# Performance work log

Hardware: AMD Instinct MI355X
Metric: run time of the kernel (lower is better)

Reference implementation:

```python
import jax, jax.numpy as jnp
import numpy as np

B, S, D = 8, 1024, 1024
H = 16
D_HEAD = D // H
RANK = 256
NC = 64
NE = 64
KC = 16  # top_k_compress
KE = 8   # top_k_expand


def setup_inputs() -> dict:
    key = jax.random.key(0)
    ks = jax.random.split(key, 9)
    rn = lambda k, sh, s=1.0: jax.random.normal(k, sh, jnp.float32) * s
    return {
        "x": rn(ks[0], (B, S, D)),
        "importance": jax.random.uniform(ks[1], (B, S), jnp.float32),
        "W_compress": rn(ks[2], (NC, D), 1.0 / np.sqrt(D)),
        "W_Q": rn(ks[3], (NE, D), 1.0 / np.sqrt(D)),
        "W_K": rn(ks[4], (NE, D), 1.0 / np.sqrt(D)),
        "W_V": rn(ks[5], (NE, D), 1.0 / np.sqrt(D)),
        "compress_neurons": rn(ks[6], (NC, D, RANK), 1.0 / np.sqrt(D)),
        "expand_pool": rn(ks[7], (NE, RANK, D), 1.0 / np.sqrt(RANK)),
        "W_O": rn(ks[8], (D, D), 1.0 / np.sqrt(D)),
    }


def _route(x, importance, W, k):
    """Per-token softmax router, importance-aggregated, top-k renormalized."""
    pref = jax.nn.softmax(jnp.einsum('bsd,nd->bsn', x, W), axis=-1)  # [B,S,n]
    w = jnp.einsum('bs,bsn->bn', importance, pref)                   # [B,n]
    w = w / (w.sum(-1, keepdims=True) + 1e-8)
    tw, ti = jax.lax.top_k(w, k)                                     # [B,k]
    tw = tw / (tw.sum(-1, keepdims=True) + 1e-8)
    return tw, ti


def reference(x, importance, W_compress, W_Q, W_K, W_V, compress_neurons, expand_pool, W_O):
    # --- GlobalRouters.get_attention_weights ---
    cw, ci = _route(x, importance, W_compress, KC)
    qw, qi = _route(x, importance, W_Q, KE)
    kw, ki = _route(x, importance, W_K, KE)
    vw, vi = _route(x, importance, W_V, KE)

    # --- NeuronCircuit.forward ---
    # gather + mix compress neurons: [B,KC,D,R] -> [B,D,R]
    shared_c = jnp.einsum('bk,bkdr->bdr', cw, compress_neurons[ci])
    h = jnp.einsum('bsd,bdr->bsr', x, shared_c)  # [B,S,R]

    eQ = jnp.einsum('bk,bkrd->brd', qw, expand_pool[qi])
    eK = jnp.einsum('bk,bkrd->brd', kw, expand_pool[ki])
    eV = jnp.einsum('bk,bkrd->brd', vw, expand_pool[vi])

    def heads(t):  # [B,S,D] -> [B,H,S,d_head]
        return t.reshape(B, S, H, D_HEAD).transpose(0, 2, 1, 3)

    Q = heads(jnp.einsum('bsr,brd->bsd', h, eQ))
    K = heads(jnp.einsum('bsr,brd->bsd', h, eK))
    V = heads(jnp.einsum('bsr,brd->bsd', h, eV))

    scale = 1.0 / np.sqrt(D_HEAD)
    scores = jnp.einsum('bhqd,bhkd->bhqk', Q, K) * scale
    causal = jnp.tril(jnp.ones((S, S), dtype=bool))
    scores = jnp.where(causal, scores, jnp.finfo(scores.dtype).min)
    attn = jax.nn.softmax(scores, axis=-1)
    out = jnp.einsum('bhqk,bhkd->bhqd', attn, V)
    out = out.transpose(0, 2, 1, 3).reshape(B, S, D)
    return jnp.einsum('bsd,ed->bse', out, W_O)  # expand_O (Linear, no bias)
```

## Files before the change

kernel.cpp:

```cpp
#include <hip/hip_runtime.h>

typedef __attribute__((ext_vector_type(8))) short short8;
typedef __attribute__((ext_vector_type(4))) short short4v;
typedef __attribute__((ext_vector_type(4))) float f32x4;
typedef unsigned short u16;
typedef unsigned int u32;

__device__ __forceinline__ float bf2f(u16 h) {
    return __uint_as_float(((u32)h) << 16);
}
__device__ __forceinline__ u16 f2bf(float f) {
    u32 u = __float_as_uint(f);
    u32 r = u + 0x7fffu + ((u >> 16) & 1u);
    return (u16)(r >> 16);
}
__device__ __forceinline__ u32 pack_bf(float a, float b) {
    return __builtin_amdgcn_perm(__float_as_uint(b), __float_as_uint(a), 0x07060302u);
}

__device__ __forceinline__ void async_copy16(const void* g, void* l) {
    __builtin_amdgcn_global_load_lds(
        (const __attribute__((address_space(1))) void*)g,
        (__attribute__((address_space(3))) void*)l, 16, 0, 0);
}

__global__ __launch_bounds__(256) void cvt_split(
    const float* __restrict__ in, u16* __restrict__ hi, u16* __restrict__ lo, int n4)
{
    int i = blockIdx.x * 256 + threadIdx.x;
    if (i >= n4) return;
    float4 v = ((const float4*)in)[i];
    short4v h, l;
    float vv[4] = {v.x, v.y, v.z, v.w};
#pragma unroll
    for (int j = 0; j < 4; j++) {
        u16 hb = f2bf(vv[j]);
        h[j] = (short)hb;
        l[j] = (short)f2bf(vv[j] - bf2f(hb));
    }
    ((short4v*)hi)[i] = h;
    ((short4v*)lo)[i] = l;
}

__global__ __launch_bounds__(256) void cvt_split_w4(
    const float* __restrict__ w0, const float* __restrict__ w1,
    const float* __restrict__ w2, const float* __restrict__ w3,
    u16* __restrict__ hi, u16* __restrict__ lo)
{
    const int r = blockIdx.x >> 6;
    const float* src = (r == 0) ? w0 : (r == 1) ? w1 : (r == 2) ? w2 : w3;
    int i = (blockIdx.x & 63) * 256 + threadIdx.x;
    float4 v = ((const float4*)src)[i];
    short4v h, l;
    float vv[4] = {v.x, v.y, v.z, v.w};
#pragma unroll
    for (int j = 0; j < 4; j++) {
        u16 hb = f2bf(vv[j]);
        h[j] = (short)hb;
        l[j] = (short)f2bf(vv[j] - bf2f(hb));
    }
    ((short4v*)(hi + (long)r * 65536))[i] = h;
    ((short4v*)(lo + (long)r * 65536))[i] = l;
}

__global__ __launch_bounds__(256) void cvt_bf(
    const float* __restrict__ in, u16* __restrict__ out, int n4)
{
    int i = blockIdx.x * 256 + threadIdx.x;
    if (i >= n4) return;
    float4 v = ((const float4*)in)[i];
    short4v h;
    h[0] = (short)f2bf(v.x); h[1] = (short)f2bf(v.y);
    h[2] = (short)f2bf(v.z); h[3] = (short)f2bf(v.w);
    ((short4v*)out)[i] = h;
}

template <typename CT>
__global__ __launch_bounds__(256) void gemm_bt(
    const u16* __restrict__ A, long lda, long bsA,
    const u16* __restrict__ Bm, long ldb, long bsB,
    CT* __restrict__ C, long ldc, long bsC, int K, float cscale)
{
    __shared__ __align__(16) u16 lsA[128 * 32];
    __shared__ __align__(16) u16 lsB[128 * 32];
    const int tid = threadIdx.x;
    const int wave = tid >> 6, lane = tid & 63;
    const int quad = lane >> 4, l15 = lane & 15;
    const int wm = wave >> 1, wn = wave & 1;
    const long m0 = (long)blockIdx.x * 128, n0 = (long)blockIdx.y * 128;
    A  += (long)blockIdx.z * bsA;
    Bm += (long)blockIdx.z * bsB;
    C  += (long)blockIdx.z * bsC;
    const int srow = lane >> 2, scol = (lane & 3) * 8;

    f32x4 acc[4][4];
#pragma unroll
    for (int i = 0; i < 4; i++)
#pragma unroll
        for (int j = 0; j < 4; j++) acc[i][j] = (f32x4){0.f, 0.f, 0.f, 0.f};

    const u16* ga0 = A + (m0 + (wave * 2 + 0) * 16 + srow) * lda + scol;
    const u16* ga1 = A + (m0 + (wave * 2 + 1) * 16 + srow) * lda + scol;
    const u16* gb0 = Bm + (n0 + (wave * 2 + 0) * 16 + srow) * ldb + scol;
    const u16* gb1 = Bm + (n0 + (wave * 2 + 1) * 16 + srow) * ldb + scol;
    u16* la0 = &lsA[(wave * 2 + 0) * 512];
    u16* la1 = &lsA[(wave * 2 + 1) * 512];
    u16* lb0 = &lsB[(wave * 2 + 0) * 512];
    u16* lb1 = &lsB[(wave * 2 + 1) * 512];

    for (int kk = 0; kk < K; kk += 32) {
        async_copy16(ga0 + kk, la0);
        async_copy16(ga1 + kk, la1);
        async_copy16(gb0 + kk, lb0);
        async_copy16(gb1 + kk, lb1);
        __syncthreads();
        short8 af[4], bf[4];
#pragma unroll
        for (int mt = 0; mt < 4; mt++)
            af[mt] = *(const short8*)&lsA[(wm * 64 + mt * 16 + l15) * 32 + quad * 8];
#pragma unroll
        for (int nt = 0; nt < 4; nt++)
            bf[nt] = *(const short8*)&lsB[(wn * 64 + nt * 16 + l15) * 32 + quad * 8];
#pragma unroll
        for (int mt = 0; mt < 4; mt++)
#pragma unroll
            for (int nt = 0; nt < 4; nt++)
                acc[mt][nt] = __builtin_amdgcn_mfma_f32_16x16x32_bf16(
                    af[mt], bf[nt], acc[mt][nt], 0, 0, 0);
        __syncthreads();
    }
#pragma unroll
    for (int mt = 0; mt < 4; mt++) {
        const long rowb = m0 + wm * 64 + mt * 16 + quad * 4;
#pragma unroll
        for (int nt = 0; nt < 4; nt++) {
            const long col = n0 + wn * 64 + nt * 16 + l15;
#pragma unroll
            for (int r = 0; r < 4; r++) {
                const float v = acc[mt][nt][r] * cscale;
                if constexpr (sizeof(CT) == 2)
                    C[(rowb + r) * ldc + col] = f2bf(v);
                else
                    C[(rowb + r) * ldc + col] = v;
            }
        }
    }
}

__global__ __launch_bounds__(256) void gemm_qkv(
    const u16* __restrict__ hbuf, const u16* __restrict__ eQT,
    const u16* __restrict__ eKT, const u16* __restrict__ eVT,
    u16* __restrict__ Qb, u16* __restrict__ Kb, u16* __restrict__ VTb)
{
    __shared__ __align__(16) u16 lsA[128 * 32];
    __shared__ __align__(16) u16 lsB[128 * 32];
    const int z = blockIdx.z;
    const int sel = z >> 3, bbz = z & 7;
    const long ab = (long)bbz * 262144;
    const u16* A  = ((sel == 2) ? eVT : hbuf) + ab;
    const u16* Bm = ((sel == 0) ? eQT : (sel == 1) ? eKT : hbuf) + ab;
    u16* C = ((sel == 0) ? Qb : (sel == 1) ? Kb : VTb) + (long)bbz * 1048576;
    const float cscale = (sel == 0) ? 0.180336880111f : 1.0f;

    const int tid = threadIdx.x;
    const int wave = tid >> 6, lane = tid & 63;
    const int quad = lane >> 4, l15 = lane & 15;
    const int wm = wave >> 1, wn = wave & 1;
    const long m0 = (long)blockIdx.x * 128, n0 = (long)blockIdx.y * 128;
    const int srow = lane >> 2, scol = (lane & 3) * 8;

    f32x4 acc[4][4];
#pragma unroll
    for (int i = 0; i < 4; i++)
#pragma unroll
        for (int j = 0; j < 4; j++) acc[i][j] = (f32x4){0.f, 0.f, 0.f, 0.f};

    const u16* ga0 = A + (m0 + (wave * 2 + 0) * 16 + srow) * 256 + scol;
    const u16* ga1 = A + (m0 + (wave * 2 + 1) * 16 + srow) * 256 + scol;
    const u16* gb0 = Bm + (n0 + (wave * 2 + 0) * 16 + srow) * 256 + scol;
    const u16* gb1 = Bm + (n0 + (wave * 2 + 1) * 16 + srow) * 256 + scol;
    u16* la0 = &lsA[(wave * 2 + 0) * 512];
    u16* la1 = &lsA[(wave * 2 + 1) * 512];
    u16* lb0 = &lsB[(wave * 2 + 0) * 512];
    u16* lb1 = &lsB[(wave * 2 + 1) * 512];

    for (int kk = 0; kk < 256; kk += 32) {
        async_copy16(ga0 + kk, la0);
        async_copy16(ga1 + kk, la1);
        async_copy16(gb0 + kk, lb0);
        async_copy16(gb1 + kk, lb1);
        __syncthreads();
        short8 af[4], bf[4];
#pragma unroll
        for (int mt = 0; mt < 4; mt++)
            af[mt] = *(const short8*)&lsA[(wm * 64 + mt * 16 + l15) * 32 + quad * 8];
#pragma unroll
        for (int nt = 0; nt < 4; nt++)
            bf[nt] = *(const short8*)&lsB[(wn * 64 + nt * 16 + l15) * 32 + quad * 8];
#pragma unroll
        for (int mt = 0; mt < 4; mt++)
#pragma unroll
            for (int nt = 0; nt < 4; nt++)
                acc[mt][nt] = __builtin_amdgcn_mfma_f32_16x16x32_bf16(
                    af[mt], bf[nt], acc[mt][nt], 0, 0, 0);
        __syncthreads();
    }
#pragma unroll
    for (int mt = 0; mt < 4; mt++) {
        const long rowb = m0 + wm * 64 + mt * 16 + quad * 4;
#pragma unroll
        for (int nt = 0; nt < 4; nt++) {
            const long col = n0 + wn * 64 + nt * 16 + l15;
#pragma unroll
            for (int r = 0; r < 4; r++)
                C[(rowb + r) * 1024 + col] = f2bf(acc[mt][nt][r] * cscale);
        }
    }
}

__global__ __launch_bounds__(256) void gemm_router(
    const u16* __restrict__ Ah, const u16* __restrict__ Al,
    const u16* __restrict__ Bh, const u16* __restrict__ Bl,
    float* __restrict__ C)
{
    __shared__ __align__(16) u16 lsA[128 * 32];
    __shared__ __align__(16) u16 lsB[128 * 32];
    const int tid = threadIdx.x;
    const int wave = tid >> 6, lane = tid & 63;
    const int quad = lane >> 4, l15 = lane & 15;
    const int wm = wave >> 1, wn = wave & 1;
    const long m0 = (long)blockIdx.x * 128, n0 = (long)blockIdx.y * 128;
    const int srow = lane >> 2, scol = (lane & 3) * 8;
    const long offA = (m0 + (wave * 2) * 16 + srow) * 1024 + scol;
    const long offB = (n0 + (wave * 2) * 16 + srow) * 1024 + scol;
    u16* la0 = &lsA[(wave * 2 + 0) * 512];
    u16* la1 = &lsA[(wave * 2 + 1) * 512];
    u16* lb0 = &lsB[(wave * 2 + 0) * 512];
    u16* lb1 = &lsB[(wave * 2 + 1) * 512];

    f32x4 acc[4][4];
#pragma unroll
    for (int i = 0; i < 4; i++)
#pragma unroll
        for (int j = 0; j < 4; j++) acc[i][j] = (f32x4){0.f, 0.f, 0.f, 0.f};

    for (int seg = 0; seg < 3; seg++) {
        const u16* A = (seg == 1) ? Al : Ah;
        const u16* B = (seg == 2) ? Bl : Bh;
        const u16* ga = A + offA;
        const u16* gb = B + offB;
        for (int kk = 0; kk < 1024; kk += 32) {
            async_copy16(ga + kk, la0);
            async_copy16(ga + 16384 + kk, la1);
            async_copy16(gb + kk, lb0);
            async_copy16(gb + 16384 + kk, lb1);
            __syncthreads();
            short8 af[4], bf[4];
#pragma unroll
            for (int mt = 0; mt < 4; mt++)
                af[mt] = *(const short8*)&lsA[(wm * 64 + mt * 16 + l15) * 32 + quad * 8];
#pragma unroll
            for (int nt = 0; nt < 4; nt++)
                bf[nt] = *(const short8*)&lsB[(wn * 64 + nt * 16 + l15) * 32 + quad * 8];
#pragma unroll
            for (int mt = 0; mt < 4; mt++)
#pragma unroll
                for (int nt = 0; nt < 4; nt++)
                    acc[mt][nt] = __builtin_amdgcn_mfma_f32_16x16x32_bf16(
                        af[mt], bf[nt], acc[mt][nt], 0, 0, 0);
            __syncthreads();
        }
    }
#pragma unroll
    for (int mt = 0; mt < 4; mt++) {
        const long rowb = m0 + wm * 64 + mt * 16 + quad * 4;
#pragma unroll
        for (int nt = 0; nt < 4; nt++) {
            const long col = n0 + wn * 64 + nt * 16 + l15;
#pragma unroll
            for (int r = 0; r < 4; r++)
                C[(rowb + r) * 256 + col] = acc[mt][nt][r];
        }
    }
}

__global__ __launch_bounds__(128) void router_agg(
    const float* __restrict__ logits, const float* __restrict__ imp,
    float* __restrict__ w_raw)
{
    __shared__ float pref[32][257];
    const int tid = threadIdx.x;
    const int tl = tid >> 2, r = tid & 3;
    const int s = blockIdx.x * 32 + tl;
    const int b = s >> 10;
    const float* lp = logits + (long)s * 256 + r * 64;
    float v[64];
#pragma unroll
    for (int i = 0; i < 16; i++) {
        float4 f = ((const float4*)lp)[i];
        v[i * 4 + 0] = f.x; v[i * 4 + 1] = f.y;
        v[i * 4 + 2] = f.z; v[i * 4 + 3] = f.w;
    }
    float mx = v[0];
#pragma unroll
    for (int i = 1; i < 64; i++) mx = fmaxf(mx, v[i]);
    float sum = 0.f;
#pragma unroll
    for (int i = 0; i < 64; i++) { v[i] = __expf(v[i] - mx); sum += v[i]; }
    const float scale = imp[s] / sum;
#pragma unroll
    for (int i = 0; i < 64; i++) pref[tl][r * 64 + i] = v[i] * scale;
    __syncthreads();
#pragma unroll
    for (int half = 0; half < 2; half++) {
        const int idx = tid + half * 128;
        const int r2 = idx >> 6, n = idx & 63;
        float acc = 0.f;
#pragma unroll 8
        for (int t = 0; t < 32; t++) acc += pref[t][r2 * 64 + n];
        atomicAdd(&w_raw[(r2 * 8 + b) * 64 + n], acc);
    }
}

__global__ void topk_kernel(const float* __restrict__ w_raw,
                            float* __restrict__ topw, int* __restrict__ topi)
{
    const int r = blockIdx.x >> 3, b = blockIdx.x & 7;
    const int lane = threadIdx.x;
    const int k = (r == 0) ? 16 : 8;
    float w = w_raw[(r * 8 + b) * 64 + lane];
    float tot = w;
    for (int o2 = 32; o2 >= 1; o2 >>= 1) tot += __shfl_xor(tot, o2);
    w = w / (tot + 1e-8f);
    __shared__ float tw[16];
    __shared__ int ti[16];
    float cur = w;
    float ssum = 0.f;
    for (int j = 0; j < k; j++) {
        float m = cur; int mi = lane;
        for (int o2 = 32; o2 >= 1; o2 >>= 1) {
            float om = __shfl_xor(m, o2); int oi = __shfl_xor(mi, o2);
            if (om > m || (om == m && oi < mi)) { m = om; mi = oi; }
        }
        if (lane == 0) { tw[j] = m; ti[j] = mi; }
        ssum += m;
        if (lane == mi) cur = -1e30f;
    }
    __syncthreads();
    if (lane < 16) {
        topw[(r * 8 + b) * 16 + lane] = (lane < k) ? tw[lane] / (ssum + 1e-8f) : 0.f;
        topi[(r * 8 + b) * 16 + lane] = (lane < k) ? ti[lane] : 0;
    }
}

__global__ __launch_bounds__(256) void gather_mix(
    const float* __restrict__ pool, const float* __restrict__ topw,
    const int* __restrict__ topi, u16* __restrict__ out,
    int I, int J, int k)
{
    __shared__ float tile[64][65];
    const int b = blockIdx.z;
    const long IJ = (long)I * J;
    const int i0 = blockIdx.x * 64, j0 = blockIdx.y * 64;
    const float* tw = topw + b * 16;
    const int* ti = topi + b * 16;
    const int tid = threadIdx.x;
    const int il = tid >> 2, jg = tid & 3;
    float acc[16];
#pragma unroll
    for (int m = 0; m < 16; m++) acc[m] = 0.f;
    for (int kk = 0; kk < k; kk++) {
        const float wgt = tw[kk];
        const long n = ti[kk];
        const float* src = pool + n * IJ + (long)(i0 + il) * J + j0 + jg * 16;
        float4 a0 = ((const float4*)src)[0];
        float4 a1 = ((const float4*)src)[1];
        float4 a2 = ((const float4*)src)[2];
        float4 a3 = ((const float4*)src)[3];
        acc[0] += wgt * a0.x;  acc[1] += wgt * a0.y;
        acc[2] += wgt * a0.z;  acc[3] += wgt * a0.w;
        acc[4] += wgt * a1.x;  acc[5] += wgt * a1.y;
        acc[6] += wgt * a1.z;  acc[7] += wgt * a1.w;
        acc[8] += wgt * a2.x;  acc[9] += wgt * a2.y;
        acc[10] += wgt * a2.z; acc[11] += wgt * a2.w;
        acc[12] += wgt * a3.x; acc[13] += wgt * a3.y;
        acc[14] += wgt * a3.z; acc[15] += wgt * a3.w;
    }
#pragma unroll
    for (int m = 0; m < 16; m++) tile[il][jg * 16 + m] = acc[m];
    __syncthreads();
    const int jl = tid >> 2, ig = tid & 3;
    short8 o0, o1;
#pragma unroll
    for (int m = 0; m < 8; m++) {
        o0[m] = (short)f2bf(tile[ig * 16 + m][jl]);
        o1[m] = (short)f2bf(tile[ig * 16 + 8 + m][jl]);
    }
    u16* dst = out + (long)b * IJ + (long)(j0 + jl) * I + i0 + ig * 16;
    *(short8*)dst = o0;
    *(short8*)(dst + 8) = o1;
}

__global__ __launch_bounds__(256) void gather_mix3(
    const float* __restrict__ pool, const float* __restrict__ topw,
    const int* __restrict__ topi, u16* __restrict__ eQT,
    u16* __restrict__ eKT, u16* __restrict__ eVT)
{
    __shared__ float tile[64][65];
    const int z = blockIdx.z;
    const int r = z >> 3, b = z & 7;
    u16* out = (r == 0) ? eQT : (r == 1) ? eKT : eVT;
    const long IJ = 262144;
    const int i0 = blockIdx.x * 64, j0 = blockIdx.y * 64;
    const float* tw = topw + (1 + r) * 128 + b * 16;
    const int* ti = topi + (1 + r) * 128 + b * 16;
    const int tid = threadIdx.x;
    const int il = tid >> 2, jg = tid & 3;
    float acc[16];
#pragma unroll
    for (int m = 0; m < 16; m++) acc[m] = 0.f;
    for (int kk = 0; kk < 8; kk++) {
        const float wgt = tw[kk];
        const long n = ti[kk];
        const float* src = pool + n * IJ + (long)(i0 + il) * 1024 + j0 + jg * 16;
        float4 a0 = ((const float4*)src)[0];
        float4 a1 = ((const float4*)src)[1];
        float4 a2 = ((const float4*)src)[2];
        float4 a3 = ((const float4*)src)[3];
        acc[0] += wgt * a0.x;  acc[1] += wgt * a0.y;
        acc[2] += wgt * a0.z;  acc[3] += wgt * a0.w;
        acc[4] += wgt * a1.x;  acc[5] += wgt * a1.y;
        acc[6] += wgt * a1.z;  acc[7] += wgt * a1.w;
        acc[8] += wgt * a2.x;  acc[9] += wgt * a2.y;
        acc[10] += wgt * a2.z; acc[11] += wgt * a2.w;
        acc[12] += wgt * a3.x; acc[13] += wgt * a3.y;
        acc[14] += wgt * a3.z; acc[15] += wgt * a3.w;
    }
#pragma unroll
    for (int m = 0; m < 16; m++) tile[il][jg * 16 + m] = acc[m];
    __syncthreads();
    const int jl = tid >> 2, ig = tid & 3;
    short8 o0, o1;
#pragma unroll
    for (int m = 0; m < 8; m++) {
        o0[m] = (short)f2bf(tile[ig * 16 + m][jl]);
        o1[m] = (short)f2bf(tile[ig * 16 + 8 + m][jl]);
    }
    u16* dst = out + (long)b * IJ + (long)(j0 + jl) * 256 + i0 + ig * 16;
    *(short8*)dst = o0;
    *(short8*)(dst + 8) = o1;
}

__global__ __launch_bounds__(256, 3) void flash_attn(
    const u16* __restrict__ Qg, const u16* __restrict__ Kg,
    const u16* __restrict__ Vt, u16* __restrict__ Og)
{
    __shared__ __align__(16) u16 plds[4][32 * 72];
    const int tid = threadIdx.x;
    const int wv = tid >> 6, lane = tid & 63;
    const int quad = lane >> 4, l15 = lane & 15;
    const int bidx = blockIdx.x;
    const int bh = bidx & 127;
    const int qt = ((7 - (bidx >> 7)) << 2) + wv;
    const int hh = bh & 15, bb = bh >> 4;
    const long SD = 1024L * 1024L;
    const u16* Qb = Qg + (long)bb * SD + hh * 64;
    const u16* Kb = Kg + (long)bb * SD + hh * 64;
    const u16* Vb = Vt + (long)bb * SD + (long)hh * 64 * 1024;
    u16* myp = plds[wv];

    const int q0 = qt * 32;

    short8 qf[2][2];
#pragma unroll
    for (int mt = 0; mt < 2; mt++)
#pragma unroll
        for (int kb = 0; kb < 2; kb++)
            qf[mt][kb] = *(const short8*)(Qb + (long)(q0 + mt * 16 + l15) * 1024 + kb * 32 + quad * 8);

    f32x4 o[2][4];
    float mrow[2] = {-3e38f, -3e38f}, lrow[2] = {0.f, 0.f};
#pragma unroll
    for (int mt = 0; mt < 2; mt++)
#pragma unroll
        for (int nt = 0; nt < 4; nt++) o[mt][nt] = (f32x4){0.f, 0.f, 0.f, 0.f};

    const int ntile = (q0 + 95) >> 6;

    for (int it = 0; it < ntile; it++) {
        const int k2 = it * 64;
        const bool last = (it == ntile - 1);
        short8 kf[4][2];
#pragma unroll
        for (int kt = 0; kt < 4; kt++)
#pragma unroll
            for (int kb = 0; kb < 2; kb++)
                kf[kt][kb] = *(const short8*)(Kb + (long)(k2 + kt * 16 + l15) * 1024 + kb * 32 + quad * 8);
        f32x4 st[4][2];
#pragma unroll
        for (int kt = 0; kt < 4; kt++)
#pragma unroll
            for (int q_ = 0; q_ < 2; q_++) {
                f32x4 z = (f32x4){0.f, 0.f, 0.f, 0.f};
                z = __builtin_amdgcn_mfma_f32_16x16x32_bf16(kf[kt][0], qf[q_][0], z, 0, 0, 0);
                z = __builtin_amdgcn_mfma_f32_16x16x32_bf16(kf[kt][1], qf[q_][1], z, 0, 0, 0);
                st[kt][q_] = z;
            }
        short8 vf[4][2];
#pragma unroll
        for (int nt = 0; nt < 4; nt++)
#pragma unroll
            for (int kh = 0; kh < 2; kh++)
                vf[nt][kh] = *(const short8*)(Vb + (long)(nt * 16 + l15) * 1024 + k2 + kh * 32 + quad * 8);
        float am[2];
#pragma unroll
        for (int q_ = 0; q_ < 2; q_++) {
            if (last) {
#pragma unroll
                for (int kt = 0; kt < 4; kt++)
#pragma unroll
                    for (int r = 0; r < 4; r++)
                        if (k2 + kt * 16 + quad * 4 + r > q0 + q_ * 16 + l15)
                            st[kt][q_][r] = -3e38f;
            }
            float cm = -3e38f;
#pragma unroll
            for (int kt = 0; kt < 4; kt++)
#pragma unroll
                for (int r = 0; r < 4; r++) cm = fmaxf(cm, st[kt][q_][r]);
            cm = fmaxf(cm, __shfl_xor(cm, 16));
            cm = fmaxf(cm, __shfl_xor(cm, 32));
            const float mn = fmaxf(mrow[q_], cm);
            am[q_] = exp2f(mrow[q_] - mn);
            mrow[q_] = mn;
            const float moff = 0.00281502f - mn;
            float rs = 0.f;
#pragma unroll
            for (int kt = 0; kt < 4; kt++) {
                float p0 = exp2f(st[kt][q_][0] + moff);
                float p1 = exp2f(st[kt][q_][1] + moff);
                float p2 = exp2f(st[kt][q_][2] + moff);
                float p3 = exp2f(st[kt][q_][3] + moff);
                rs += (p0 + p1) + (p2 + p3);
                u32 w0 = pack_bf(p0, p1);
                u32 w1 = pack_bf(p2, p3);
                *(uint2*)&myp[(q_ * 16 + l15) * 72 + kt * 16 + quad * 4] = make_uint2(w0, w1);
            }
            rs += __shfl_xor(rs, 16);
            rs += __shfl_xor(rs, 32);
            lrow[q_] = lrow[q_] * am[q_] + rs;
        }
        float av[2][4];
#pragma unroll
        for (int mt = 0; mt < 2; mt++)
#pragma unroll
            for (int r = 0; r < 4; r++)
                av[mt][r] = __shfl(am[mt], quad * 4 + r);
        asm volatile("s_waitcnt lgkmcnt(0)" ::: "memory");
        short8 pf0[2], pf1[2];
#pragma unroll
        for (int kh = 0; kh < 2; kh++) {
            pf0[kh] = *(const short8*)&myp[(l15) * 72 + kh * 32 + quad * 8];
            pf1[kh] = *(const short8*)&myp[(16 + l15) * 72 + kh * 32 + quad * 8];
        }
#pragma unroll
        for (int mt = 0; mt < 2; mt++)
#pragma unroll
            for (int nt = 0; nt < 4; nt++)
#pragma unroll
                for (int r = 0; r < 4; r++) o[mt][nt][r] *= av[mt][r];
#pragma unroll
        for (int nt = 0; nt < 4; nt++)
#pragma unroll
            for (int kh = 0; kh < 2; kh++) {
                o[0][nt] = __builtin_amdgcn_mfma_f32_16x16x32_bf16(pf0[kh], vf[nt][kh], o[0][nt], 0, 0, 0);
                o[1][nt] = __builtin_amdgcn_mfma_f32_16x16x32_bf16(pf1[kh], vf[nt][kh], o[1][nt], 0, 0, 0);
            }
    }
#pragma unroll
    for (int mt = 0; mt < 2; mt++)
#pragma unroll
        for (int r = 0; r < 4; r++) {
            const float li = 1.0f / __shfl(lrow[mt], quad * 4 + r);
            const long row = q0 + mt * 16 + quad * 4 + r;
#pragma unroll
            for (int nt = 0; nt < 4; nt++)
                Og[(long)bb * SD + row * 1024 + hh * 64 + nt * 16 + l15] =
                    f2bf(o[mt][nt][r] * li);
        }
}

extern "C" void kernel_launch(void* const* d_in, const int* in_sizes, int n_in,
                              void* d_out, int out_size, void* d_ws, size_t ws_size,
                              hipStream_t stream)
{
    const float* x   = (const float*)d_in[0];
    const float* imp = (const float*)d_in[1];
    const float* cn  = (const float*)d_in[6];
    const float* ep  = (const float*)d_in[7];
    const float* Wo  = (const float*)d_in[8];
    float* outp = (float*)d_out;
    char* ws = (char*)d_ws;

    u16* xh = (u16*)d_out;
    u16* xl = xh + 8388608;

    u16*   Wh     = (u16*)(ws + 0);
    u16*   Wl     = (u16*)(ws + 524288);
    u16*   Wobf   = (u16*)(ws + 1048576);
    float* w_raw  = (float*)(ws + 3145728);
    float* topw   = (float*)(ws + 3153920);
    int*   topi   = (int*)(ws + 3155968);
    float* logits = (float*)(ws + 4194304);
    u16*   scT    = (u16*)(ws + 12582912);
    u16*   eQT    = (u16*)(ws + 16777216);
    u16*   Kb     = (u16*)(ws + 4194304);
    u16*   hbuf   = (u16*)(ws + 20971520);
    u16*   eKT    = (u16*)(ws + 25165824);
    u16*   eVT    = (u16*)(ws + 29360128);
    u16*   Qb     = (u16*)(ws + 33554432);
    u16*   VTb    = (u16*)(ws + 50331648);
    u16*   aout   = (u16*)(ws + 67108864);

    cvt_split<<<dim3(8192), 256, 0, stream>>>(x, xh, xl, 2097152);
    cvt_split_w4<<<dim3(256), 256, 0, stream>>>(
        (const float*)d_in[2], (const float*)d_in[3],
        (const float*)d_in[4], (const float*)d_in[5], Wh, Wl);
    cvt_bf<<<dim3(1024), 256, 0, stream>>>(Wo, Wobf, 262144);
    hipMemsetAsync(w_raw, 0, 4 * 8 * 64 * 4, stream);

    gemm_router<<<dim3(64, 2, 1), 256, 0, stream>>>(xh, xl, Wh, Wl, logits);
    router_agg<<<dim3(256), 128, 0, stream>>>(logits, imp, w_raw);
    topk_kernel<<<dim3(32), 64, 0, stream>>>(w_raw, topw, topi);
    gather_mix<<<dim3(16, 4, 8), 256, 0, stream>>>(cn, topw + 0 * 128, topi + 0 * 128, scT, 1024, 256, 16);
    gather_mix3<<<dim3(4, 16, 24), 256, 0, stream>>>(ep, topw, topi, eQT, eKT, eVT);
    gemm_bt<u16><<<dim3(8, 2, 8), 256, 0, stream>>>(
        xh, 1024, 1048576, scT, 1024, 262144, hbuf, 256, 262144, 1024, 1.0f);
    gemm_qkv<<<dim3(8, 8, 24), 256, 0, stream>>>(hbuf, eQT, eKT, eVT, Qb, Kb, VTb);
    flash_attn<<<dim3(1024), 256, 0, stream>>>(Qb, Kb, VTb, aout);
    gemm_bt<float><<<dim3(64, 8, 1), 256, 0, stream>>>(
        aout, 1024, 0, Wobf, 1024, 0, outp, 1024, 0, 1024, 1.0f);
}
```

Baseline: 448.2 us.

## Split router GEMM segments across blocks and keep attention P in registers

The three split-precision router GEMM passes now run as separate grid slices along z, writing three partial logit buffers that router_agg sums. This triples the number of blocks for a grid that was only 128 blocks, at the cost of extra logit memory traffic. Flash attention now prefetches the next K tile during the current tile's compute, builds the P operand with cross-lane shuffles instead of an LDS round trip, and uses a tree reduction for the row max. These changes target latency and LDS traffic in the attention loop and add shuffle instructions and register pressure in exchange.

Result: no change. 439.5 us (-2.0%).

```diff
diff --git a/kernel.cpp b/kernel.cpp
--- a/kernel.cpp
+++ b/kernel.cpp
@@ -5,6 +5,7 @@
 typedef __attribute__((ext_vector_type(4))) float f32x4;
 typedef unsigned short u16;
 typedef unsigned int u32;
+typedef __attribute__((ext_vector_type(4))) u32 u32x4;
 
 __device__ __forceinline__ float bf2f(u16 h) {
     return __uint_as_float(((u32)h) << 16);
@@ -16,6 +17,10 @@
 }
 __device__ __forceinline__ u32 pack_bf(float a, float b) {
     return __builtin_amdgcn_perm(__float_as_uint(b), __float_as_uint(a), 0x07060302u);
+}
+__device__ __forceinline__ short8 u4_to_s8(u32 a, u32 b, u32 c, u32 d) {
+    u32x4 t = (u32x4){a, b, c, d};
+    return __builtin_bit_cast(short8, t);
 }
 
 __device__ __forceinline__ void async_copy16(const void* g, void* l) {
@@ -221,18 +226,22 @@
 __global__ __launch_bounds__(256) void gemm_router(
     const u16* __restrict__ Ah, const u16* __restrict__ Al,
     const u16* __restrict__ Bh, const u16* __restrict__ Bl,
-    float* __restrict__ C)
+    float* __restrict__ C0, float* __restrict__ C1, float* __restrict__ C2)
 {
     __shared__ __align__(16) u16 lsA[128 * 32];
     __shared__ __align__(16) u16 lsB[128 * 32];
+    const int seg = blockIdx.z;
+    const u16* A = (seg == 1) ? Al : Ah;
+    const u16* B = (seg == 2) ? Bl : Bh;
+    float* C = (seg == 0) ? C0 : (seg == 1) ? C1 : C2;
     const int tid = threadIdx.x;
     const int wave = tid >> 6, lane = tid & 63;
     const int quad = lane >> 4, l15 = lane & 15;
     const int wm = wave >> 1, wn = wave & 1;
     const long m0 = (long)blockIdx.x * 128, n0 = (long)blockIdx.y * 128;
     const int srow = lane >> 2, scol = (lane & 3) * 8;
-    const long offA = (m0 + (wave * 2) * 16 + srow) * 1024 + scol;
-    const long offB = (n0 + (wave * 2) * 16 + srow) * 1024 + scol;
+    const u16* ga = A + (m0 + (wave * 2) * 16 + srow) * 1024 + scol;
+    const u16* gb = B + (n0 + (wave * 2) * 16 + srow) * 1024 + scol;
     u16* la0 = &lsA[(wave * 2 + 0) * 512];
     u16* la1 = &lsA[(wave * 2 + 1) * 512];
     u16* lb0 = &lsB[(wave * 2 + 0) * 512];
@@ -244,32 +253,26 @@
 #pragma unroll
         for (int j = 0; j < 4; j++) acc[i][j] = (f32x4){0.f, 0.f, 0.f, 0.f};
 
-    for (int seg = 0; seg < 3; seg++) {
-        const u16* A = (seg == 1) ? Al : Ah;
-        const u16* B = (seg == 2) ? Bl : Bh;
-        const u16* ga = A + offA;
-        const u16* gb = B + offB;
-        for (int kk = 0; kk < 1024; kk += 32) {
-            async_copy16(ga + kk, la0);
-            async_copy16(ga + 16384 + kk, la1);
-            async_copy16(gb + kk, lb0);
-            async_copy16(gb + 16384 + kk, lb1);
-            __syncthreads();
-            short8 af[4], bf[4];
-#pragma unroll
-            for (int mt = 0; mt < 4; mt++)
-                af[mt] = *(const short8*)&lsA[(wm * 64 + mt * 16 + l15) * 32 + quad * 8];
+    for (int kk = 0; kk < 1024; kk += 32) {
+        async_copy16(ga + kk, la0);
+        async_copy16(ga + 16384 + kk, la1);
+        async_copy16(gb + kk, lb0);
+        async_copy16(gb + 16384 + kk, lb1);
+        __syncthreads();
+        short8 af[4], bf[4];
+#pragma unroll
+        for (int mt = 0; mt < 4; mt++)
+            af[mt] = *(const short8*)&lsA[(wm * 64 + mt * 16 + l15) * 32 + quad * 8];
+#pragma unroll
+        for (int nt = 0; nt < 4; nt++)
+            bf[nt] = *(const short8*)&lsB[(wn * 64 + nt * 16 + l15) * 32 + quad * 8];
+#pragma unroll
+        for (int mt = 0; mt < 4; mt++)
 #pragma unroll
             for (int nt = 0; nt < 4; nt++)
-                bf[nt] = *(const short8*)&lsB[(wn * 64 + nt * 16 + l15) * 32 + quad * 8];
-#pragma unroll
-            for (int mt = 0; mt < 4; mt++)
-#pragma unroll
-                for (int nt = 0; nt < 4; nt++)
-                    acc[mt][nt] = __builtin_amdgcn_mfma_f32_16x16x32_bf16(
-                        af[mt], bf[nt], acc[mt][nt], 0, 0, 0);
-            __syncthreads();
-        }
+                acc[mt][nt] = __builtin_amdgcn_mfma_f32_16x16x32_bf16(
+                    af[mt], bf[nt], acc[mt][nt], 0, 0, 0);
+        __syncthreads();
     }
 #pragma unroll
     for (int mt = 0; mt < 4; mt++) {
@@ -285,7 +288,8 @@
 }
 
 __global__ __launch_bounds__(128) void router_agg(
-    const float* __restrict__ logits, const float* __restrict__ imp,
+    const float* __restrict__ l0, const float* __restrict__ l1,
+    const float* __restrict__ l2, const float* __restrict__ imp,
     float* __restrict__ w_raw)
 {
     __shared__ float pref[32][257];
@@ -293,13 +297,17 @@
     const int tl = tid >> 2, r = tid & 3;
     const int s = blockIdx.x * 32 + tl;
     const int b = s >> 10;
-    const float* lp = logits + (long)s * 256 + r * 64;
+    const long off = (long)s * 256 + r * 64;
     float v[64];
 #pragma unroll
     for (int i = 0; i < 16; i++) {
-        float4 f = ((const float4*)lp)[i];
-        v[i * 4 + 0] = f.x; v[i * 4 + 1] = f.y;
-        v[i * 4 + 2] = f.z; v[i * 4 + 3] = f.w;
+        float4 f0 = ((const float4*)(l0 + off))[i];
+        float4 f1 = ((const float4*)(l1 + off))[i];
+        float4 f2 = ((const float4*)(l2 + off))[i];
+        v[i * 4 + 0] = f0.x + f1.x + f2.x;
+        v[i * 4 + 1] = f0.y + f1.y + f2.y;
+        v[i * 4 + 2] = f0.z + f1.z + f2.z;
+        v[i * 4 + 3] = f0.w + f1.w + f2.w;
     }
     float mx = v[0];
 #pragma unroll
@@ -455,7 +463,6 @@
     const u16* __restrict__ Qg, const u16* __restrict__ Kg,
     const u16* __restrict__ Vt, u16* __restrict__ Og)
 {
-    __shared__ __align__(16) u16 plds[4][32 * 72];
     const int tid = threadIdx.x;
     const int wv = tid >> 6, lane = tid & 63;
     const int quad = lane >> 4, l15 = lane & 15;
@@ -467,7 +474,6 @@
     const u16* Qb = Qg + (long)bb * SD + hh * 64;
     const u16* Kb = Kg + (long)bb * SD + hh * 64;
     const u16* Vb = Vt + (long)bb * SD + (long)hh * 64 * 1024;
-    u16* myp = plds[wv];
 
     const int q0 = qt * 32;
 
@@ -486,16 +492,20 @@
         for (int nt = 0; nt < 4; nt++) o[mt][nt] = (f32x4){0.f, 0.f, 0.f, 0.f};
 
     const int ntile = (q0 + 95) >> 6;
+    short8 kf[4][2];
+#pragma unroll
+    for (int kt = 0; kt < 4; kt++)
+#pragma unroll
+        for (int kb = 0; kb < 2; kb++)
+            kf[kt][kb] = *(const short8*)(Kb + (long)(kt * 16 + l15) * 1024 + kb * 32 + quad * 8);
+
+    const int sl01 = l15 + ((((quad << 1) + 0) & 3) << 4);
+    const int sl23 = l15 + ((((quad << 1) + 1) & 3) << 4);
+    const bool loquad = (quad < 2);
 
     for (int it = 0; it < ntile; it++) {
         const int k2 = it * 64;
         const bool last = (it == ntile - 1);
-        short8 kf[4][2];
-#pragma unroll
-        for (int kt = 0; kt < 4; kt++)
-#pragma unroll
-            for (int kb = 0; kb < 2; kb++)
-                kf[kt][kb] = *(const short8*)(Kb + (long)(k2 + kt * 16 + l15) * 1024 + kb * 32 + quad * 8);
         f32x4 st[4][2];
 #pragma unroll
         for (int kt = 0; kt < 4; kt++)
@@ -506,6 +516,13 @@
                 z = __builtin_amdgcn_mfma_f32_16x16x32_bf16(kf[kt][1], qf[q_][1], z, 0, 0, 0);
                 st[kt][q_] = z;
             }
+        if (it + 1 < ntile) {
+#pragma unroll
+            for (int kt = 0; kt < 4; kt++)
+#pragma unroll
+                for (int kb = 0; kb < 2; kb++)
+                    kf[kt][kb] = *(const short8*)(Kb + (long)(k2 + 64 + kt * 16 + l15) * 1024 + kb * 32 + quad * 8);
+        }
         short8 vf[4][2];
 #pragma unroll
         for (int nt = 0; nt < 4; nt++)
@@ -513,6 +530,7 @@
             for (int kh = 0; kh < 2; kh++)
                 vf[nt][kh] = *(const short8*)(Vb + (long)(nt * 16 + l15) * 1024 + k2 + kh * 32 + quad * 8);
         float am[2];
+        u32 pa[2][2][4];
 #pragma unroll
         for (int q_ = 0; q_ < 2; q_++) {
             if (last) {
@@ -523,32 +541,42 @@
                         if (k2 + kt * 16 + quad * 4 + r > q0 + q_ * 16 + l15)
                             st[kt][q_][r] = -3e38f;
             }
-            float cm = -3e38f;
-#pragma unroll
-            for (int kt = 0; kt < 4; kt++)
-#pragma unroll
-                for (int r = 0; r < 4; r++) cm = fmaxf(cm, st[kt][q_][r]);
+            float t0 = fmaxf(fmaxf(st[0][q_][0], st[0][q_][1]), fmaxf(st[0][q_][2], st[0][q_][3]));
+            float t1 = fmaxf(fmaxf(st[1][q_][0], st[1][q_][1]), fmaxf(st[1][q_][2], st[1][q_][3]));
+            float t2 = fmaxf(fmaxf(st[2][q_][0], st[2][q_][1]), fmaxf(st[2][q_][2], st[2][q_][3]));
+            float t3 = fmaxf(fmaxf(st[3][q_][0], st[3][q_][1]), fmaxf(st[3][q_][2], st[3][q_][3]));
+            float cm = fmaxf(fmaxf(t0, t1), fmaxf(t2, t3));
             cm = fmaxf(cm, __shfl_xor(cm, 16));
             cm = fmaxf(cm, __shfl_xor(cm, 32));
             const float mn = fmaxf(mrow[q_], cm);
             am[q_] = exp2f(mrow[q_] - mn);
             mrow[q_] = mn;
             const float moff = 0.00281502f - mn;
-            float rs = 0.f;
+            u32 w[4][2];
+            float s4[4];
 #pragma unroll
             for (int kt = 0; kt < 4; kt++) {
                 float p0 = exp2f(st[kt][q_][0] + moff);
                 float p1 = exp2f(st[kt][q_][1] + moff);
                 float p2 = exp2f(st[kt][q_][2] + moff);
                 float p3 = exp2f(st[kt][q_][3] + moff);
-                rs += (p0 + p1) + (p2 + p3);
-                u32 w0 = pack_bf(p0, p1);
-                u32 w1 = pack_bf(p2, p3);
-                *(uint2*)&myp[(q_ * 16 + l15) * 72 + kt * 16 + quad * 4] = make_uint2(w0, w1);
+                s4[kt] = (p0 + p1) + (p2 + p3);
+                w[kt][0] = pack_bf(p0, p1);
+                w[kt][1] = pack_bf(p2, p3);
             }
+            float rs = (s4[0] + s4[1]) + (s4[2] + s4[3]);
             rs += __shfl_xor(rs, 16);
             rs += __shfl_xor(rs, 32);
             lrow[q_] = lrow[q_] * am[q_] + rs;
+#pragma unroll
+            for (int kh = 0; kh < 2; kh++)
+#pragma unroll
+                for (int c = 0; c < 4; c++) {
+                    const int sl = (c < 2) ? sl01 : sl23;
+                    u32 vA = (u32)__shfl((int)w[2 * kh + 0][c & 1], sl);
+                    u32 vB = (u32)__shfl((int)w[2 * kh + 1][c & 1], sl);
+                    pa[q_][kh][c] = loquad ? vA : vB;
+                }
         }
         float av[2][4];
 #pragma unroll
@@ -556,19 +584,18 @@
 #pragma unroll
             for (int r = 0; r < 4; r++)
                 av[mt][r] = __shfl(am[mt], quad * 4 + r);
-        asm volatile("s_waitcnt lgkmcnt(0)" ::: "memory");
+#pragma unroll
+        for (int mt = 0; mt < 2; mt++)
+#pragma unroll
+            for (int nt = 0; nt < 4; nt++)
+#pragma unroll
+                for (int r = 0; r < 4; r++) o[mt][nt][r] *= av[mt][r];
         short8 pf0[2], pf1[2];
 #pragma unroll
         for (int kh = 0; kh < 2; kh++) {
-            pf0[kh] = *(const short8*)&myp[(l15) * 72 + kh * 32 + quad * 8];
-            pf1[kh] = *(const short8*)&myp[(16 + l15) * 72 + kh * 32 + quad * 8];
-        }
-#pragma unroll
-        for (int mt = 0; mt < 2; mt++)
-#pragma unroll
-            for (int nt = 0; nt < 4; nt++)
-#pragma unroll
-                for (int r = 0; r < 4; r++) o[mt][nt][r] *= av[mt][r];
+            pf0[kh] = u4_to_s8(pa[0][kh][0], pa[0][kh][1], pa[0][kh][2], pa[0][kh][3]);
+            pf1[kh] = u4_to_s8(pa[1][kh][0], pa[1][kh][1], pa[1][kh][2], pa[1][kh][3]);
+        }
 #pragma unroll
         for (int nt = 0; nt < 4; nt++)
 #pragma unroll
@@ -611,7 +638,9 @@
     float* w_raw  = (float*)(ws + 3145728);
     float* topw   = (float*)(ws + 3153920);
     int*   topi   = (int*)(ws + 3155968);
-    float* logits = (float*)(ws + 4194304);
+    float* logit0 = (float*)(ws + 4194304);
+    float* logit1 = (float*)(ws + 33554432);
+    float* logit2 = (float*)(ws + 41943040);
     u16*   scT    = (u16*)(ws + 12582912);
     u16*   eQT    = (u16*)(ws + 16777216);
     u16*   Kb     = (u16*)(ws + 4194304);
@@ -629,8 +658,9 @@
     cvt_bf<<<dim3(1024), 256, 0, stream>>>(Wo, Wobf, 262144);
     hipMemsetAsync(w_raw, 0, 4 * 8 * 64 * 4, stream);
 
-    gemm_router<<<dim3(64, 2, 1), 256, 0, stream>>>(xh, xl, Wh, Wl, logits);
-    router_agg<<<dim3(256), 128, 0, stream>>>(logits, imp, w_raw);
+    gemm_router<<<dim3(64, 2, 3), 256, 0, stream>>>(
+        xh, xl, Wh, Wl, logit0, logit1, logit2);
+    router_agg<<<dim3(256), 128, 0, stream>>>(logit0, logit1, logit2, imp, w_raw);
     topk_kernel<<<dim3(32), 64, 0, stream>>>(w_raw, topw, topi);
     gather_mix<<<dim3(16, 4, 8), 256, 0, stream>>>(cn, topw + 0 * 128, topi + 0 * 128, scT, 1024, 256, 16);
     gather_mix3<<<dim3(4, 16, 24), 256, 0, stream>>>(ep, topw, topi, eQT, eKT, eVT);
```
